# Performance work log

Hardware: AMD Instinct MI355X
Metric: run time of the kernel (lower is better)

Reference implementation:

```python
import jax, jax.numpy as jnp
import numpy as np

N, F_IN, H, MH = 50000, 128, 128, 256
E = 800000

def _lin_init(key, out_d, in_d, bias=True):
    k1, k2 = jax.random.split(key)
    bound = 1.0 / np.sqrt(in_d)
    W = jax.random.uniform(k1, (out_d, in_d), minval=-bound, maxval=bound, dtype=jnp.float32)
    if bias:
        b = jax.random.uniform(k2, (out_d,), minval=-bound, maxval=bound, dtype=jnp.float32)
        return W, b
    return W, None

def setup_inputs() -> dict:
    key = jax.random.key(0)
    ks = jax.random.split(key, 8)
    x = jax.random.normal(ks[0], (N, F_IN), dtype=jnp.float32)
    edge_index = jax.random.randint(ks[1], (2, E), 0, N, dtype=jnp.int64)
    W1l, b1l = _lin_init(ks[2], H, F_IN, bias=True)   # SAGEConv1 neighbor lin (with bias)
    W1r, _ = _lin_init(ks[3], H, F_IN, bias=False)    # SAGEConv1 root lin (no bias)
    W2l, b2l = _lin_init(ks[4], H, H, bias=True)
    W2r, _ = _lin_init(ks[5], H, H, bias=False)
    Wm1, bm1 = _lin_init(ks[6], MH, 2 * H, bias=True)
    Wm2, bm2 = _lin_init(ks[7], 1, MH, bias=True)
    return {"x": x, "edge_index": edge_index,
            "W1l": W1l, "b1l": b1l, "W1r": W1r,
            "W2l": W2l, "b2l": b2l, "W2r": W2r,
            "Wm1": Wm1, "bm1": bm1, "Wm2": Wm2, "bm2": bm2}

def _sage_conv(x, src, dst, Wl, bl, Wr, num_nodes):
    # mean-aggregate messages x[src] at dst, then lin_l(agg) + lin_r(x)
    agg = jax.ops.segment_sum(x[src], dst, num_segments=num_nodes)
    cnt = jax.ops.segment_sum(jnp.ones((src.shape[0],), x.dtype), dst, num_segments=num_nodes)
    agg = agg / jnp.maximum(cnt, 1.0)[:, None]
    return agg @ Wl.T + bl + x @ Wr.T

def reference(x, edge_index, W1l, b1l, W1r, W2l, b2l, W2r, Wm1, bm1, Wm2, bm2):
    src, dst = edge_index[0], edge_index[1]
    n = x.shape[0]
    h = jax.nn.relu(_sage_conv(x, src, dst, W1l, b1l, W1r, n))
    # dropout is identity in eval mode
    h = jax.nn.relu(_sage_conv(h, src, dst, W2l, b2l, W2r, n))
    ef = jnp.concatenate([h[src], h[dst]], axis=-1)  # [E, 2H]
    out = jax.nn.relu(ef @ Wm1.T + bm1) @ Wm2.T + bm2
    return out.reshape(-1)
```

## Files before the change

kernel.cpp:

```cpp
#include <hip/hip_runtime.h>
#include <hip/hip_bf16.h>

#define NN 50000
#define F 128
#define EE 800000
#define MHD 256
#define CAP 44

typedef __attribute__((ext_vector_type(8))) short bf16x8;
typedef __attribute__((ext_vector_type(4))) float f32x4;

__device__ __forceinline__ float b2f(unsigned short u) {
    union { unsigned int i; float f; } v; v.i = ((unsigned)u) << 16; return v.f;
}
__device__ __forceinline__ unsigned short f2b(float f) {
    unsigned int x = __float_as_uint(f);
    unsigned int r = x + 0x7fffu + ((x >> 16) & 1u);
    return (unsigned short)(r >> 16);
}

__global__ __launch_bounds__(256) void cast_zero_kernel(
    const float* __restrict__ x,
    const float* __restrict__ W1l, const float* __restrict__ W1r,
    const float* __restrict__ W2l, const float* __restrict__ W2r,
    const float* __restrict__ Wm1, const float* __restrict__ Wm2,
    unsigned short* __restrict__ xb, unsigned short* __restrict__ wb,
    int* __restrict__ cntp, float* __restrict__ w2p) {
    int bid = blockIdx.x;
    if (bid < 6250) {
        int i = (bid * 256 + threadIdx.x) * 4;
        float4 v = *(const float4*)(x + i);
        ushort4 o; o.x = f2b(v.x); o.y = f2b(v.y); o.z = f2b(v.z); o.w = f2b(v.w);
        *(ushort4*)(xb + i) = o;
    } else if (bid < 6378) {
        int i = ((bid - 6250) * 256 + threadIdx.x) * 4;
        unsigned short o[4];
        if (i < 32768) {
            const float* p = (i < 16384) ? (W1l + i) : (W1r + (i - 16384));
            float4 v = *(const float4*)p;
            o[0] = f2b(v.x); o[1] = f2b(v.y); o[2] = f2b(v.z); o[3] = f2b(v.w);
        } else if (i < 65536) {
            int local = i - 32768;
            const float* M = (local < 16384) ? W2l : W2r;
            int lm = local & 16383;
            int n = lm >> 7, kp = lm & 127;
#pragma unroll
            for (int t = 0; t < 4; t++) {
                int k = ((kp + t) & 7) * 16 + ((kp + t) >> 3);
                o[t] = f2b(M[n * 128 + k]);
            }
        } else {
            int local = i - 65536;
            int n = local >> 8, k2 = local & 255;
            int half = k2 >> 7, kp = k2 & 127;
#pragma unroll
            for (int t = 0; t < 4; t++) {
                int k = half * 128 + ((kp + t) & 7) * 16 + ((kp + t) >> 3);
                o[t] = f2b(Wm1[n * 256 + k]);
            }
        }
        *(ushort4*)(wb + i) = *(ushort4*)o;
    } else if (bid < 7160) {
        int idx = ((bid - 6378) * 256 + threadIdx.x) * 4;
        if (idx < NN * 16) *(int4*)(cntp + idx) = (int4){0, 0, 0, 0};
    } else {
        int t = threadIdx.x;
        w2p[t] = Wm2[(t & 15) * 16 + (t >> 4)];
    }
}

__global__ __launch_bounds__(256) void cvt_fill_kernel(
    const int* __restrict__ ei, int* __restrict__ cntp,
    unsigned short* __restrict__ slots) {
    __shared__ int isI64;
    if (threadIdx.x == 0) {
        int z = 0;
        for (int i = 1; i < 128; i += 2) z |= ei[i];
        isI64 = (z == 0) ? 1 : 0;
    }
    __syncthreads();
    int e = blockIdx.x * 256 + threadIdx.x;
    if (e >= EE) return;
    int s, d;
    if (isI64) {
        const long long* e64 = (const long long*)ei;
        s = (int)e64[e];
        d = (int)e64[EE + e];
    } else {
        s = ei[e];
        d = ei[EE + e];
    }
    int pos = atomicAdd(&cntp[d << 4], 1);
    if (pos < CAP) {
        unsigned short* sp = slots + (size_t)d * (CAP * 3) + pos * 3;
        sp[0] = (unsigned short)s;
        sp[1] = (unsigned short)(e & 0xffff);
        sp[2] = (unsigned short)((unsigned)e >> 16);
    }
}

__global__ __launch_bounds__(256) void sage_layer_kernel(
    const unsigned short* __restrict__ xin,
    const unsigned short* __restrict__ slots, const int* __restrict__ cntp,
    int* __restrict__ cnt2,
    const unsigned short* __restrict__ W1, const unsigned short* __restrict__ W2,
    const float* __restrict__ bias,
    unsigned short* __restrict__ out) {
    __shared__ unsigned short lds[4][16][136];
    int wave = threadIdx.x >> 6, lane = threadIdx.x & 63;
    int m0 = (blockIdx.x * 4 + wave) * 16;

    int g = lane >> 4, l16 = lane & 15, col8 = l16 * 8;
    for (int batch = 0; batch < 4; batch++) {
        int node = m0 + batch * 4 + g;
        int n = 0, ctrue = 0;
        const unsigned short* sp = slots;
        if (node < NN) {
            ctrue = cntp[node << 4];
            n = (ctrue < CAP) ? ctrue : CAP;
            sp = slots + (size_t)node * (CAP * 3);
            if (l16 == 0) cnt2[node] = ctrue;
        }
        float a[8] = {0,0,0,0,0,0,0,0};
        float b[8] = {0,0,0,0,0,0,0,0};
        int j = 0;
        for (; j + 7 < n; j += 8) {
            int s0 = sp[(j + 0) * 3], s1 = sp[(j + 1) * 3];
            int s2 = sp[(j + 2) * 3], s3 = sp[(j + 3) * 3];
            int s4 = sp[(j + 4) * 3], s5 = sp[(j + 5) * 3];
            int s6 = sp[(j + 6) * 3], s7 = sp[(j + 7) * 3];
            bf16x8 v0 = *(const bf16x8*)(xin + (size_t)s0 * F + col8);
            bf16x8 v1 = *(const bf16x8*)(xin + (size_t)s1 * F + col8);
            bf16x8 v2 = *(const bf16x8*)(xin + (size_t)s2 * F + col8);
            bf16x8 v3 = *(const bf16x8*)(xin + (size_t)s3 * F + col8);
            bf16x8 v4 = *(const bf16x8*)(xin + (size_t)s4 * F + col8);
            bf16x8 v5 = *(const bf16x8*)(xin + (size_t)s5 * F + col8);
            bf16x8 v6 = *(const bf16x8*)(xin + (size_t)s6 * F + col8);
            bf16x8 v7 = *(const bf16x8*)(xin + (size_t)s7 * F + col8);
            for (int i = 0; i < 8; i++)
                a[i] += (b2f((unsigned short)v0[i]) + b2f((unsigned short)v1[i]))
                      + (b2f((unsigned short)v2[i]) + b2f((unsigned short)v3[i]));
            for (int i = 0; i < 8; i++)
                b[i] += (b2f((unsigned short)v4[i]) + b2f((unsigned short)v5[i]))
                      + (b2f((unsigned short)v6[i]) + b2f((unsigned short)v7[i]));
        }
        for (; j + 3 < n; j += 4) {
            int s0 = sp[(j + 0) * 3], s1 = sp[(j + 1) * 3];
            int s2 = sp[(j + 2) * 3], s3 = sp[(j + 3) * 3];
            bf16x8 v0 = *(const bf16x8*)(xin + (size_t)s0 * F + col8);
            bf16x8 v1 = *(const bf16x8*)(xin + (size_t)s1 * F + col8);
            bf16x8 v2 = *(const bf16x8*)(xin + (size_t)s2 * F + col8);
            bf16x8 v3 = *(const bf16x8*)(xin + (size_t)s3 * F + col8);
            for (int i = 0; i < 8; i++)
                a[i] += (b2f((unsigned short)v0[i]) + b2f((unsigned short)v1[i]))
                      + (b2f((unsigned short)v2[i]) + b2f((unsigned short)v3[i]));
        }
        for (; j < n; j++) {
            int s0 = sp[j * 3];
            bf16x8 v0 = *(const bf16x8*)(xin + (size_t)s0 * F + col8);
            for (int i = 0; i < 8; i++) a[i] += b2f((unsigned short)v0[i]);
        }
        float inv = 1.0f / fmaxf((float)ctrue, 1.0f);
        unsigned short o[8];
        for (int i = 0; i < 8; i++) o[i] = f2b((a[i] + b[i]) * inv);
        *(bf16x8*)&lds[wave][batch * 4 + g][col8] = *(bf16x8*)o;
    }
    __syncthreads();

    int c = lane & 15, q = lane >> 4;
    f32x4 acc[8];
    for (int nt = 0; nt < 8; nt++) {
        float b = bias[nt * 16 + c];
        acc[nt] = (f32x4){b, b, b, b};
    }
    int mrow = m0 + c; if (mrow > NN - 1) mrow = NN - 1;
    for (int op = 0; op < 2; op++) {
        const unsigned short* W = op ? W2 : W1;
        for (int kb = 0; kb < 4; kb++) {
            bf16x8 a;
            if (op == 0) a = *(const bf16x8*)&lds[wave][c][kb * 32 + q * 8];
            else         a = *(const bf16x8*)(xin + (size_t)mrow * F + kb * 32 + q * 8);
            for (int nt = 0; nt < 8; nt++) {
                bf16x8 b = *(const bf16x8*)(W + (size_t)(nt * 16 + c) * F + kb * 32 + q * 8);
                acc[nt] = __builtin_amdgcn_mfma_f32_16x16x32_bf16(a, b, acc[nt], 0, 0, 0);
            }
        }
    }
#pragma unroll
    for (int r = 0; r < 4; r++) {
        int node = m0 + q * 4 + r;
        if (node < NN) {
            unsigned short o[8];
#pragma unroll
            for (int nt = 0; nt < 8; nt++) o[nt] = f2b(fmaxf(acc[nt][r], 0.0f));
            *(bf16x8*)(out + (size_t)node * F + c * 8) = *(bf16x8*)o;
        }
    }
}

__global__ __launch_bounds__(256) void pq_gemm_kernel(
    const unsigned short* __restrict__ h,
    const unsigned short* __restrict__ wmb,
    const float* __restrict__ bm1,
    unsigned short* __restrict__ PQ) {
    int wave = threadIdx.x >> 6, lane = threadIdx.x & 63;
    int c = lane & 15, q = lane >> 4;
    int half = wave >> 1, ntBase = (wave & 1) * 8;
    int m0 = blockIdx.x * 32;
    int mr0 = m0 + c;      if (mr0 > NN - 1) mr0 = NN - 1;
    int mr1 = m0 + 16 + c; if (mr1 > NN - 1) mr1 = NN - 1;
    f32x4 acc0[8], acc1[8];
#pragma unroll
    for (int nt = 0; nt < 8; nt++) {
        float b = half ? bm1[(ntBase + nt) * 16 + c] : 0.0f;
        acc0[nt] = (f32x4){b, b, b, b};
        acc1[nt] = (f32x4){b, b, b, b};
    }
#pragma unroll
    for (int kb = 0; kb < 4; kb++) {
        bf16x8 a0 = *(const bf16x8*)(h + (size_t)mr0 * F + kb * 32 + q * 8);
        bf16x8 a1 = *(const bf16x8*)(h + (size_t)mr1 * F + kb * 32 + q * 8);
#pragma unroll
        for (int nt = 0; nt < 8; nt++) {
            bf16x8 b = *(const bf16x8*)(wmb + (size_t)((ntBase + nt) * 16 + c) * 256 + half * 128 + kb * 32 + q * 8);
            acc0[nt] = __builtin_amdgcn_mfma_f32_16x16x32_bf16(a0, b, acc0[nt], 0, 0, 0);
            acc1[nt] = __builtin_amdgcn_mfma_f32_16x16x32_bf16(a1, b, acc1[nt], 0, 0, 0);
        }
    }
#pragma unroll
    for (int r = 0; r < 4; r++) {
        int node0 = m0 + q * 4 + r;
        if (node0 < NN) {
            unsigned short o[8];
#pragma unroll
            for (int nt = 0; nt < 8; nt++) o[nt] = f2b(acc0[nt][r]);
            *(bf16x8*)(PQ + (size_t)node0 * 512 + half * 256 + c * 16 + ntBase) = *(bf16x8*)o;
        }
        int node1 = m0 + 16 + q * 4 + r;
        if (node1 < NN) {
            unsigned short o[8];
#pragma unroll
            for (int nt = 0; nt < 8; nt++) o[nt] = f2b(acc1[nt][r]);
            *(bf16x8*)(PQ + (size_t)node1 * 512 + half * 256 + c * 16 + ntBase) = *(bf16x8*)o;
        }
    }
}

__global__ __launch_bounds__(256) void edge_dot_kernel(
    const unsigned short* __restrict__ PQ,
    const unsigned short* __restrict__ slots, const int* __restrict__ cnt2,
    const float* __restrict__ w2p, const float* __restrict__ bm2,
    float* __restrict__ out) {
    int wave = threadIdx.x >> 6, lane = threadIdx.x & 63;
    int node = blockIdx.x * 4 + wave;
    if (node >= NN) return;
    int g = lane >> 4, l16 = lane & 15;
    int col = l16 * 16;
    float w2f[16], qf[16];
    *(float4*)(w2f + 0)  = *(const float4*)(w2p + col + 0);
    *(float4*)(w2f + 4)  = *(const float4*)(w2p + col + 4);
    *(float4*)(w2f + 8)  = *(const float4*)(w2p + col + 8);
    *(float4*)(w2f + 12) = *(const float4*)(w2p + col + 12);
    {
        bf16x8 q0 = *(const bf16x8*)(PQ + (size_t)node * 512 + 256 + col);
        bf16x8 q1 = *(const bf16x8*)(PQ + (size_t)node * 512 + 256 + col + 8);
#pragma unroll
        for (int i = 0; i < 8; i++) { qf[i] = b2f((unsigned short)q0[i]); qf[8 + i] = b2f((unsigned short)q1[i]); }
    }
    float b2 = bm2[0];
    int ctrue = cnt2[node];
    int n = (ctrue < CAP) ? ctrue : CAP;
    const unsigned short* sp = slots + (size_t)node * (CAP * 3);
    int j = g;
    for (; j + 4 < n; j += 8) {
        int s0 = sp[j * 3],       s1 = sp[(j + 4) * 3];
        int eid0 = sp[j * 3 + 1] | ((int)sp[j * 3 + 2] << 16);
        int eid1 = sp[(j + 4) * 3 + 1] | ((int)sp[(j + 4) * 3 + 2] << 16);
        uint4 a0 = *(const uint4*)(PQ + (size_t)s0 * 512 + col);
        uint4 a1 = *(const uint4*)(PQ + (size_t)s0 * 512 + col + 8);
        uint4 c0 = *(const uint4*)(PQ + (size_t)s1 * 512 + col);
        uint4 c1 = *(const uint4*)(PQ + (size_t)s1 * 512 + col + 8);
        float t0 = 0.f, t1 = 0.f;
        unsigned int w0[8] = {a0.x, a0.y, a0.z, a0.w, a1.x, a1.y, a1.z, a1.w};
        unsigned int w1[8] = {c0.x, c0.y, c0.z, c0.w, c1.x, c1.y, c1.z, c1.w};
#pragma unroll
        for (int i = 0; i < 8; i++) {
            float lo0 = __uint_as_float(w0[i] << 16);
            float hi0 = __uint_as_float(w0[i] & 0xffff0000u);
            float lo1 = __uint_as_float(w1[i] << 16);
            float hi1 = __uint_as_float(w1[i] & 0xffff0000u);
            t0 += fmaxf(lo0 + qf[2 * i], 0.f) * w2f[2 * i]
                + fmaxf(hi0 + qf[2 * i + 1], 0.f) * w2f[2 * i + 1];
            t1 += fmaxf(lo1 + qf[2 * i], 0.f) * w2f[2 * i]
                + fmaxf(hi1 + qf[2 * i + 1], 0.f) * w2f[2 * i + 1];
        }
        t0 += __shfl_xor(t0, 1);  t1 += __shfl_xor(t1, 1);
        t0 += __shfl_xor(t0, 2);  t1 += __shfl_xor(t1, 2);
        t0 += __shfl_xor(t0, 4);  t1 += __shfl_xor(t1, 4);
        t0 += __shfl_xor(t0, 8);  t1 += __shfl_xor(t1, 8);
        if (l16 == 0) { out[eid0] = t0 + b2; out[eid1] = t1 + b2; }
    }
    for (; j < n; j += 4) {
        int s0 = sp[j * 3];
        int eid0 = sp[j * 3 + 1] | ((int)sp[j * 3 + 2] << 16);
        uint4 a0 = *(const uint4*)(PQ + (size_t)s0 * 512 + col);
        uint4 a1 = *(const uint4*)(PQ + (size_t)s0 * 512 + col + 8);
        unsigned int w0[8] = {a0.x, a0.y, a0.z, a0.w, a1.x, a1.y, a1.z, a1.w};
        float t = 0.f;
#pragma unroll
        for (int i = 0; i < 8; i++) {
            float lo = __uint_as_float(w0[i] << 16);
            float hi = __uint_as_float(w0[i] & 0xffff0000u);
            t += fmaxf(lo + qf[2 * i], 0.f) * w2f[2 * i]
               + fmaxf(hi + qf[2 * i + 1], 0.f) * w2f[2 * i + 1];
        }
        t += __shfl_xor(t, 1);
        t += __shfl_xor(t, 2);
        t += __shfl_xor(t, 4);
        t += __shfl_xor(t, 8);
        if (l16 == 0) out[eid0] = t + b2;
    }
}

extern "C" void kernel_launch(void* const* d_in, const int* in_sizes, int n_in,
                              void* d_out, int out_size, void* d_ws, size_t ws_size,
                              hipStream_t stream) {
    const float* x   = (const float*)d_in[0];
    const int*   ei  = (const int*)d_in[1];
    const float* W1l = (const float*)d_in[2];
    const float* b1l = (const float*)d_in[3];
    const float* W1r = (const float*)d_in[4];
    const float* W2l = (const float*)d_in[5];
    const float* b2l = (const float*)d_in[6];
    const float* W2r = (const float*)d_in[7];
    const float* Wm1 = (const float*)d_in[8];
    const float* bm1 = (const float*)d_in[9];
    const float* Wm2 = (const float*)d_in[10];
    const float* bm2 = (const float*)d_in[11];

    char* ws = (char*)d_ws;
    unsigned short* PQ    = (unsigned short*)(ws);
    unsigned short* xb    = (unsigned short*)(ws);
    unsigned short* h1    = (unsigned short*)(ws + 12800000);
    int*            cntp  = (int*)(ws + 25600000);
    unsigned short* wb    = (unsigned short*)(ws + 51200000);
    float*          w2p   = (float*)(ws + 51462144);
    int*            cnt2  = (int*)(ws + 51463168);
    unsigned short* slots = (unsigned short*)(ws + 51663168);
    unsigned short* h2    = (unsigned short*)(ws + 64863168);
    float*          outp  = (float*)d_out;

    const unsigned short* w1l_b  = wb;
    const unsigned short* w1r_b  = wb + 16384;
    const unsigned short* w2l_p  = wb + 32768;
    const unsigned short* w2r_p  = wb + 49152;
    const unsigned short* wm1_p  = wb + 65536;

    cast_zero_kernel<<<7161, 256, 0, stream>>>(x, W1l, W1r, W2l, W2r, Wm1, Wm2, xb, wb, cntp, w2p);
    cvt_fill_kernel<<<3125, 256, 0, stream>>>(ei, cntp, slots);

    sage_layer_kernel<<<782, 256, 0, stream>>>(xb, slots, cntp, cnt2, w1l_b, w1r_b, b1l, h1);
    sage_layer_kernel<<<782, 256, 0, stream>>>(h1, slots, cntp, cnt2, w2l_p, w2r_p, b2l, h2);
    pq_gemm_kernel<<<1563, 256, 0, stream>>>(h2, wm1_p, bm1, PQ);
    edge_dot_kernel<<<12500, 256, 0, stream>>>(PQ, slots, cnt2, w2p, bm2, outp);
}
```

Baseline: 376.7 us.

## Merge prep and edge-fill into one cooperative kernel; widen PQ GEMM tile

The cast/zero kernel and the edge bucket-fill kernel are merged into a single cooperative grid-stride kernel. A grid-wide sync separates the two phases, which removes one launch. The PQ GEMM now computes 64 rows per block instead of 32, so each weight fragment load feeds four MFMAs and half as many blocks are launched. The grid sync and fixed grid size of 1024 limit parallelism in the edge-fill phase. The larger accumulator set raises register pressure in the GEMM.

```diff
diff --git a/kernel.cpp b/kernel.cpp
--- a/kernel.cpp
+++ b/kernel.cpp
@@ -1,5 +1,8 @@
 #include <hip/hip_runtime.h>
 #include <hip/hip_bf16.h>
+#include <hip/hip_cooperative_groups.h>
+
+namespace cg = cooperative_groups;
 
 #define NN 50000
 #define F 128
@@ -19,59 +22,61 @@
     return (unsigned short)(r >> 16);
 }
 
-__global__ __launch_bounds__(256) void cast_zero_kernel(
+#define P1_UNITS 1833024
+__global__ __launch_bounds__(256) void prep_kernel(
     const float* __restrict__ x,
     const float* __restrict__ W1l, const float* __restrict__ W1r,
     const float* __restrict__ W2l, const float* __restrict__ W2r,
     const float* __restrict__ Wm1, const float* __restrict__ Wm2,
+    const int* __restrict__ ei,
     unsigned short* __restrict__ xb, unsigned short* __restrict__ wb,
-    int* __restrict__ cntp, float* __restrict__ w2p) {
-    int bid = blockIdx.x;
-    if (bid < 6250) {
-        int i = (bid * 256 + threadIdx.x) * 4;
-        float4 v = *(const float4*)(x + i);
-        ushort4 o; o.x = f2b(v.x); o.y = f2b(v.y); o.z = f2b(v.z); o.w = f2b(v.w);
-        *(ushort4*)(xb + i) = o;
-    } else if (bid < 6378) {
-        int i = ((bid - 6250) * 256 + threadIdx.x) * 4;
-        unsigned short o[4];
-        if (i < 32768) {
-            const float* p = (i < 16384) ? (W1l + i) : (W1r + (i - 16384));
-            float4 v = *(const float4*)p;
-            o[0] = f2b(v.x); o[1] = f2b(v.y); o[2] = f2b(v.z); o[3] = f2b(v.w);
-        } else if (i < 65536) {
-            int local = i - 32768;
-            const float* M = (local < 16384) ? W2l : W2r;
-            int lm = local & 16383;
-            int n = lm >> 7, kp = lm & 127;
-#pragma unroll
-            for (int t = 0; t < 4; t++) {
-                int k = ((kp + t) & 7) * 16 + ((kp + t) >> 3);
-                o[t] = f2b(M[n * 128 + k]);
+    int* __restrict__ cntp, float* __restrict__ w2p,
+    unsigned short* __restrict__ slots) {
+    int tid = blockIdx.x * 256 + threadIdx.x;
+    int stride = gridDim.x * 256;
+    for (int u = tid; u < P1_UNITS; u += stride) {
+        if (u < 1600000) {
+            int i = u * 4;
+            float4 v = *(const float4*)(x + i);
+            ushort4 o; o.x = f2b(v.x); o.y = f2b(v.y); o.z = f2b(v.z); o.w = f2b(v.w);
+            *(ushort4*)(xb + i) = o;
+        } else if (u < 1632768) {
+            int i = (u - 1600000) * 4;
+            unsigned short o[4];
+            if (i < 32768) {
+                const float* p = (i < 16384) ? (W1l + i) : (W1r + (i - 16384));
+                float4 v = *(const float4*)p;
+                o[0] = f2b(v.x); o[1] = f2b(v.y); o[2] = f2b(v.z); o[3] = f2b(v.w);
+            } else if (i < 65536) {
+                int local = i - 32768;
+                const float* M = (local < 16384) ? W2l : W2r;
+                int lm = local & 16383;
+                int n = lm >> 7, kp = lm & 127;
+#pragma unroll
+                for (int t = 0; t < 4; t++) {
+                    int k = ((kp + t) & 7) * 16 + ((kp + t) >> 3);
+                    o[t] = f2b(M[n * 128 + k]);
+                }
+            } else {
+                int local = i - 65536;
+                int n = local >> 8, k2 = local & 255;
+                int half = k2 >> 7, kp = k2 & 127;
+#pragma unroll
+                for (int t = 0; t < 4; t++) {
+                    int k = half * 128 + ((kp + t) & 7) * 16 + ((kp + t) >> 3);
+                    o[t] = f2b(Wm1[n * 256 + k]);
+                }
             }
+            *(ushort4*)(wb + i) = *(ushort4*)o;
+        } else if (u < 1832768) {
+            int idx = (u - 1632768) * 4;
+            *(int4*)(cntp + idx) = (int4){0, 0, 0, 0};
         } else {
-            int local = i - 65536;
-            int n = local >> 8, k2 = local & 255;
-            int half = k2 >> 7, kp = k2 & 127;
-#pragma unroll
-            for (int t = 0; t < 4; t++) {
-                int k = half * 128 + ((kp + t) & 7) * 16 + ((kp + t) >> 3);
-                o[t] = f2b(Wm1[n * 256 + k]);
-            }
-        }
-        *(ushort4*)(wb + i) = *(ushort4*)o;
-    } else if (bid < 7160) {
-        int idx = ((bid - 6378) * 256 + threadIdx.x) * 4;
-        if (idx < NN * 16) *(int4*)(cntp + idx) = (int4){0, 0, 0, 0};
-    } else {
-        int t = threadIdx.x;
-        w2p[t] = Wm2[(t & 15) * 16 + (t >> 4)];
-    }
-}
-
-__global__ __launch_bounds__(256) void cvt_fill_kernel(
-    const int* __restrict__ ei, int* __restrict__ cntp,
-    unsigned short* __restrict__ slots) {
+            int t = u - 1832768;
+            w2p[t] = Wm2[(t & 15) * 16 + (t >> 4)];
+        }
+    }
+    cg::this_grid().sync();
     __shared__ int isI64;
     if (threadIdx.x == 0) {
         int z = 0;
@@ -79,23 +84,23 @@
         isI64 = (z == 0) ? 1 : 0;
     }
     __syncthreads();
-    int e = blockIdx.x * 256 + threadIdx.x;
-    if (e >= EE) return;
-    int s, d;
-    if (isI64) {
-        const long long* e64 = (const long long*)ei;
-        s = (int)e64[e];
-        d = (int)e64[EE + e];
-    } else {
-        s = ei[e];
-        d = ei[EE + e];
-    }
-    int pos = atomicAdd(&cntp[d << 4], 1);
-    if (pos < CAP) {
-        unsigned short* sp = slots + (size_t)d * (CAP * 3) + pos * 3;
-        sp[0] = (unsigned short)s;
-        sp[1] = (unsigned short)(e & 0xffff);
-        sp[2] = (unsigned short)((unsigned)e >> 16);
+    for (int e = tid; e < EE; e += stride) {
+        int s, d;
+        if (isI64) {
+            const long long* e64 = (const long long*)ei;
+            s = (int)e64[e];
+            d = (int)e64[EE + e];
+        } else {
+            s = ei[e];
+            d = ei[EE + e];
+        }
+        int pos = atomicAdd(&cntp[d << 4], 1);
+        if (pos < CAP) {
+            unsigned short* sp = slots + (size_t)d * (CAP * 3) + pos * 3;
+            sp[0] = (unsigned short)s;
+            sp[1] = (unsigned short)(e & 0xffff);
+            sp[2] = (unsigned short)((unsigned)e >> 16);
+        }
     }
 }
 
@@ -206,42 +211,61 @@
     int wave = threadIdx.x >> 6, lane = threadIdx.x & 63;
     int c = lane & 15, q = lane >> 4;
     int half = wave >> 1, ntBase = (wave & 1) * 8;
-    int m0 = blockIdx.x * 32;
+    int m0 = blockIdx.x * 64;
     int mr0 = m0 + c;      if (mr0 > NN - 1) mr0 = NN - 1;
     int mr1 = m0 + 16 + c; if (mr1 > NN - 1) mr1 = NN - 1;
-    f32x4 acc0[8], acc1[8];
+    int mr2 = m0 + 32 + c; if (mr2 > NN - 1) mr2 = NN - 1;
+    int mr3 = m0 + 48 + c; if (mr3 > NN - 1) mr3 = NN - 1;
+    f32x4 acc0[8], acc1[8], acc2[8], acc3[8];
 #pragma unroll
     for (int nt = 0; nt < 8; nt++) {
         float b = half ? bm1[(ntBase + nt) * 16 + c] : 0.0f;
         acc0[nt] = (f32x4){b, b, b, b};
         acc1[nt] = (f32x4){b, b, b, b};
+        acc2[nt] = (f32x4){b, b, b, b};
+        acc3[nt] = (f32x4){b, b, b, b};
     }
 #pragma unroll
     for (int kb = 0; kb < 4; kb++) {
         bf16x8 a0 = *(const bf16x8*)(h + (size_t)mr0 * F + kb * 32 + q * 8);
         bf16x8 a1 = *(const bf16x8*)(h + (size_t)mr1 * F + kb * 32 + q * 8);
+        bf16x8 a2 = *(const bf16x8*)(h + (size_t)mr2 * F + kb * 32 + q * 8);
+        bf16x8 a3 = *(const bf16x8*)(h + (size_t)mr3 * F + kb * 32 + q * 8);
 #pragma unroll
         for (int nt = 0; nt < 8; nt++) {
             bf16x8 b = *(const bf16x8*)(wmb + (size_t)((ntBase + nt) * 16 + c) * 256 + half * 128 + kb * 32 + q * 8);
             acc0[nt] = __builtin_amdgcn_mfma_f32_16x16x32_bf16(a0, b, acc0[nt], 0, 0, 0);
             acc1[nt] = __builtin_amdgcn_mfma_f32_16x16x32_bf16(a1, b, acc1[nt], 0, 0, 0);
+            acc2[nt] = __builtin_amdgcn_mfma_f32_16x16x32_bf16(a2, b, acc2[nt], 0, 0, 0);
+            acc3[nt] = __builtin_amdgcn_mfma_f32_16x16x32_bf16(a3, b, acc3[nt], 0, 0, 0);
         }
     }
 #pragma unroll
     for (int r = 0; r < 4; r++) {
-        int node0 = m0 + q * 4 + r;
-        if (node0 < NN) {
-            unsigned short o[8];
+        int n0 = m0 + q * 4 + r;
+        int n1 = m0 + 16 + q * 4 + r;
+        int n2 = m0 + 32 + q * 4 + r;
+        int n3 = m0 + 48 + q * 4 + r;
+        unsigned short o[8];
+        if (n0 < NN) {
 #pragma unroll
             for (int nt = 0; nt < 8; nt++) o[nt] = f2b(acc0[nt][r]);
-            *(bf16x8*)(PQ + (size_t)node0 * 512 + half * 256 + c * 16 + ntBase) = *(bf16x8*)o;
-        }
-        int node1 = m0 + 16 + q * 4 + r;
-        if (node1 < NN) {
-            unsigned short o[8];
+            *(bf16x8*)(PQ + (size_t)n0 * 512 + half * 256 + c * 16 + ntBase) = *(bf16x8*)o;
+        }
+        if (n1 < NN) {
 #pragma unroll
             for (int nt = 0; nt < 8; nt++) o[nt] = f2b(acc1[nt][r]);
-            *(bf16x8*)(PQ + (size_t)node1 * 512 + half * 256 + c * 16 + ntBase) = *(bf16x8*)o;
+            *(bf16x8*)(PQ + (size_t)n1 * 512 + half * 256 + c * 16 + ntBase) = *(bf16x8*)o;
+        }
+        if (n2 < NN) {
+#pragma unroll
+            for (int nt = 0; nt < 8; nt++) o[nt] = f2b(acc2[nt][r]);
+            *(bf16x8*)(PQ + (size_t)n2 * 512 + half * 256 + c * 16 + ntBase) = *(bf16x8*)o;
+        }
+        if (n3 < NN) {
+#pragma unroll
+            for (int nt = 0; nt < 8; nt++) o[nt] = f2b(acc3[nt][r]);
+            *(bf16x8*)(PQ + (size_t)n3 * 512 + half * 256 + c * 16 + ntBase) = *(bf16x8*)o;
         }
     }
 }
@@ -356,11 +380,18 @@
     const unsigned short* w2r_p  = wb + 49152;
     const unsigned short* wm1_p  = wb + 65536;
 
-    cast_zero_kernel<<<7161, 256, 0, stream>>>(x, W1l, W1r, W2l, W2r, Wm1, Wm2, xb, wb, cntp, w2p);
-    cvt_fill_kernel<<<3125, 256, 0, stream>>>(ei, cntp, slots);
+    {
+        void* args[] = {
+            (void*)&x, (void*)&W1l, (void*)&W1r, (void*)&W2l, (void*)&W2r,
+            (void*)&Wm1, (void*)&Wm2, (void*)&ei,
+            (void*)&xb, (void*)&wb, (void*)&cntp, (void*)&w2p, (void*)&slots
+        };
+        hipLaunchCooperativeKernel((const void*)prep_kernel, dim3(1024), dim3(256),
+                                   args, 0, stream);
+    }
 
     sage_layer_kernel<<<782, 256, 0, stream>>>(xb, slots, cntp, cnt2, w1l_b, w1r_b, b1l, h1);
     sage_layer_kernel<<<782, 256, 0, stream>>>(h1, slots, cntp, cnt2, w2l_p, w2r_p, b2l, h2);
-    pq_gemm_kernel<<<1563, 256, 0, stream>>>(h2, wm1_p, bm1, PQ);
+    pq_gemm_kernel<<<782, 256, 0, stream>>>(h2, wm1_p, bm1, PQ);
     edge_dot_kernel<<<12500, 256, 0, stream>>>(PQ, slots, cnt2, w2p, bm2, outp);
 }
```

Result: slower. 476.5 us (+26.5%).
